# Performance work log

Hardware: AMD Instinct MI355X
Metric: run time of the kernel (lower is better)

Reference implementation:

```python
import jax, jax.numpy as jnp
import numpy as np

NUM_GENES = 5000
EMBED = 64
HID = 64
FEATS = 64
SLOPE = 0.01  # nn.LeakyReLU default
BN_EPS = 1e-5


def setup_inputs() -> dict:
    key = jax.random.key(0)
    ks = jax.random.split(key, 20)
    N, E = 40000, 1280000
    def w(k, shape):
        return jax.random.normal(k, shape, dtype=jnp.float32) * 0.05
    inp = {
        "x": jax.random.normal(ks[0], (N, FEATS), dtype=jnp.float32),
        "edge_index": jax.random.randint(ks[1], (2, E), 0, N, dtype=jnp.int64),
        # pre_mp Linear(num_feats, hidden)
        "W_pre": w(ks[2], (FEATS, HID)), "b_pre": w(ks[3], (HID,)),
        # conv 0 MLP: Linear->LeakyReLU->Linear
        "c0_W1": w(ks[4], (HID, HID)), "c0_b1": w(ks[5], (HID,)),
        "c0_W2": w(ks[6], (HID, HID)), "c0_b2": w(ks[7], (HID,)),
        # bn 0 (only bns[0] is used since last conv has no bn)
        "bn0_g": jnp.ones((HID,), jnp.float32), "bn0_b": jnp.zeros((HID,), jnp.float32),
        # conv 1 MLP
        "c1_W1": w(ks[8], (HID, HID)), "c1_b1": w(ks[9], (HID,)),
        "c1_W2": w(ks[10], (HID, HID)), "c1_b2": w(ks[11], (HID,)),
        # post_mp: Linear(hid,hid)->LeakyReLU->Linear(hid,embed)
        "Wp1": w(ks[12], (HID, HID)), "bp1": w(ks[13], (HID,)),
        "Wp2": w(ks[14], (HID, EMBED)), "bp2": w(ks[15], (EMBED,)),
    }
    return inp


def _gin_conv(x, src, dst, W1, b1, W2, b2):
    # GINConv, eps=0: MLP(x + sum_{j in N(i)} x_j)
    agg = jax.ops.segment_sum(x[src], dst, num_segments=x.shape[0])
    h = x + agg
    h = jax.nn.leaky_relu(h @ W1 + b1, SLOPE) @ W2 + b2
    return h


def _batchnorm(h, g, b):
    mu = h.mean(axis=0)
    var = ((h - mu) ** 2).mean(axis=0)  # biased, training-mode BN
    return (h - mu) * jax.lax.rsqrt(var + BN_EPS) * g + b


def reference(x, edge_index, W_pre, b_pre, c0_W1, c0_b1, c0_W2, c0_b2,
              bn0_g, bn0_b, c1_W1, c1_b1, c1_W2, c1_b2, Wp1, bp1, Wp2, bp2):
    src, dst = edge_index[0], edge_index[1]
    h = x @ W_pre + b_pre                                  # [N, HID]
    h = _gin_conv(h, src, dst, c0_W1, c0_b1, c0_W2, c0_b2)
    h = _batchnorm(h, bn0_g, bn0_b)
    h = _gin_conv(h, src, dst, c1_W1, c1_b1, c1_W2, c1_b2)  # last conv, no bn
    h = jax.nn.leaky_relu(h @ Wp1 + bp1, SLOPE) @ Wp2 + bp2  # [N, EMBED]
    # flatten + split into per-graph chunks of num_genes*embed, then stack
    return h.reshape(-1, NUM_GENES * EMBED)                 # [B, 5000*64]
```

## Files before the change

### kernel.cpp

```cpp
#include <hip/hip_runtime.h>
#include <hip/hip_fp16.h>

constexpr float SLOPE  = 0.01f;
constexpr float BN_EPS = 1e-5f;
constexpr int   CAP    = 96;
constexpr int   CLAMP  = 80;
constexpr int   NXCD   = 8;
constexpr int   EPB    = 2048;
constexpr int   BSH    = 7;
constexpr int   BINN   = 128;
constexpr int   MAXNB  = 320;
constexpr int   RCAP   = 24;
constexpr int   SUBCAP = 768;

__device__ inline void acc8(const uint4& v, float* a) {
    float2 f;
    f = __half22float2(*(const __half2*)&v.x); a[0] += f.x; a[1] += f.y;
    f = __half22float2(*(const __half2*)&v.y); a[2] += f.x; a[3] += f.y;
    f = __half22float2(*(const __half2*)&v.z); a[4] += f.x; a[5] += f.y;
    f = __half22float2(*(const __half2*)&v.w); a[6] += f.x; a[7] += f.y;
}

__global__ void k_linear_h(const float* __restrict__ x, const float* __restrict__ W,
                           const float* __restrict__ bias, __half* __restrict__ H0, int total) {
    int gid = blockIdx.x * blockDim.x + threadIdx.x;
    if (gid >= total) return;
    int n = gid >> 6, f = gid & 63;
    const float* row = x + (size_t)n * 64;
    float acc = bias[f];
#pragma unroll
    for (int k = 0; k < 64; ++k) acc = fmaf(row[k], W[k * 64 + f], acc);
    H0[gid] = __float2half(acc);
}

__global__ void k_binA(const int* __restrict__ src, const int* __restrict__ dst,
                       int* __restrict__ cursors, unsigned int* __restrict__ binArr,
                       int E, int NB) {
    __shared__ int lcnt[MAXNB];
    __shared__ int gb[MAXNB];
    __shared__ unsigned int lrec[MAXNB][RCAP];
    int bid = blockIdx.x, tid = threadIdx.x;
    int xcd = bid & (NXCD - 1);
    for (int i = tid; i < NB; i += 256) lcnt[i] = 0;
    __syncthreads();
    int base = bid * EPB;
#pragma unroll
    for (int i = 0; i < EPB / 256; ++i) {
        int e = base + i * 256 + tid;
        if (e < E) {
            int d = dst[e];
            int s = src[e];
            int bin = d >> BSH;
            unsigned int rec = ((unsigned int)s << BSH) | (unsigned int)(d & (BINN - 1));
            int pos = atomicAdd(&lcnt[bin], 1);
            if (pos < RCAP) lrec[bin][pos] = rec;
        }
    }
    __syncthreads();
    for (int b = tid; b < NB; b += 256) {
        int m = min(lcnt[b], RCAP);
        gb[b] = (m > 0) ? atomicAdd(&cursors[xcd * NB + b], m) : 0;
    }
    __syncthreads();
    int wid = tid >> 6, lane = tid & 63;
    for (int b = wid; b < NB; b += 4) {
        int m = min(lcnt[b], RCAP);
        if (m == 0) continue;
        int gbase = gb[b];
        unsigned int* dp = binArr + ((size_t)(xcd * NB + b)) * SUBCAP;
        for (int i = lane; i < m; i += 64) {
            int p = gbase + i;
            if (p < SUBCAP) dp[p] = lrec[b][i];
        }
    }
}

__global__ void k_binB(const int* __restrict__ cursors, const unsigned int* __restrict__ binArr,
                       int NB, int* __restrict__ cnt, unsigned short* __restrict__ ssrc, int N) {
    __shared__ int lcnt[BINN];
    __shared__ unsigned short lbkt[BINN][CAP];
    int b = blockIdx.x, tid = threadIdx.x;
    if (tid < BINN) lcnt[tid] = 0;
    __syncthreads();
#pragma unroll
    for (int xx = 0; xx < NXCD; ++xx) {
        int m = min(cursors[xx * NB + b], SUBCAP);
        const unsigned int* arr = binArr + ((size_t)(xx * NB + b)) * SUBCAP;
        for (int i = tid; i < m; i += 256) {
            unsigned int rec = arr[i];
            int dl = rec & (BINN - 1);
            int pos = atomicAdd(&lcnt[dl], 1);
            if (pos < CAP) lbkt[dl][pos] = (unsigned short)(rec >> BSH);
        }
    }
    __syncthreads();
    int n0 = b << BSH;
    int nn = min(BINN, N - n0);
    if (nn <= 0) return;
    if (tid < nn) cnt[n0 + tid] = lcnt[tid];
    const unsigned int* lb32 = (const unsigned int*)lbkt;
    unsigned int* gb32 = (unsigned int*)(ssrc + (size_t)n0 * CAP);
    int tot32 = nn * (CAP / 2);
    for (int i = tid; i < tot32; i += 256) gb32[i] = lb32[i];
}

#define GLD(j) \
    uint4 vA##j, vB##j; \
    { int jA = sidx[g][((j) << 4) + sub]; \
      int jB = sidx[g][((j) << 4) + 8 + sub]; \
      vA##j = in16[(size_t)jA * 8 + q]; \
      vB##j = in16[(size_t)jB * 8 + q]; }
#define GACC(j) do { acc8(vA##j, a); acc8(vB##j, a); } while (0)

__device__ inline float mlp_layer_lds(const unsigned int* __restrict__ Ws,
                                      const float* __restrict__ rowp, int lane, float bias) {
    float a = bias;
#pragma unroll
    for (int k0 = 0; k0 < 16; ++k0) {
        float4 r = *(const float4*)&rowp[k0 * 4];
        unsigned int wa = Ws[(2 * k0) * 64 + lane];
        unsigned int wb = Ws[(2 * k0 + 1) * 64 + lane];
        float2 fa = __half22float2(*(const __half2*)&wa);
        float2 fb = __half22float2(*(const __half2*)&wb);
        a = fmaf(r.x, fa.x, a);
        a = fmaf(r.y, fa.y, a);
        a = fmaf(r.z, fb.x, a);
        a = fmaf(r.w, fb.y, a);
    }
    return a;
}

template <bool BN_IN, bool DO_POST, typename TO>
__global__ void k_conv10(const __half* __restrict__ in, const int* __restrict__ cnt,
                         const unsigned short* __restrict__ ssrc,
                         const float* __restrict__ stats, const float* __restrict__ gm,
                         const float* __restrict__ bt, float invN,
                         const float* __restrict__ W1, const float* __restrict__ b1,
                         const float* __restrict__ W2, const float* __restrict__ b2,
                         const float* __restrict__ Wp1, const float* __restrict__ bp1,
                         const float* __restrict__ Wp2, const float* __restrict__ bp2,
                         TO* __restrict__ out, int N, int nblk) {
    constexpr int NMAT = DO_POST ? 4 : 2;
    __shared__ unsigned int Ws[NMAT][2048];
    __shared__ unsigned short sidx[4][CAP];
    __shared__ float row[4][64];
    __shared__ float t[4][64];
    __shared__ float csc[64], csh[64];

    int tid = threadIdx.x;
    {
        const float* mats[NMAT];
        mats[0] = W1; mats[1] = W2;
        if constexpr (DO_POST) { mats[2] = Wp1; mats[3] = Wp2; }
#pragma unroll
        for (int m = 0; m < NMAT; ++m) {
            const float* Wm = mats[m];
#pragma unroll
            for (int it = 0; it < 8; ++it) {
                int idx = it * 256 + tid;
                int k2 = idx >> 6, ln = idx & 63;
                float w0 = Wm[(2 * k2) * 64 + ln];
                float w1 = Wm[(2 * k2 + 1) * 64 + ln];
                __half2 h = __floats2half2_rn(w0, w1);
                Ws[m][idx] = *(unsigned int*)&h;
            }
        }
    }
    if constexpr (BN_IN) {
        if (tid < 64) {
            float mu  = stats[tid] * invN;
            float var = stats[64 + tid] * invN - mu * mu;
            float sc  = rsqrtf(var + BN_EPS) * gm[tid];
            csc[tid] = sc;
            csh[tid] = bt[tid] - mu * sc;
        }
    }
    __syncthreads();

    int bid = blockIdx.x;
    int q8 = nblk / NXCD, r8 = nblk % NXCD;
    int xcd = bid % NXCD, sl = bid / NXCD;
    int wg = (xcd < r8 ? xcd * (q8 + 1) : r8 * (q8 + 1) + (xcd - r8) * q8) + sl;
    int n0 = wg * 4;

    int lane = tid & 63, g = tid >> 6;
    int n = n0 + g;
    bool act = n < N;
    int sub = lane >> 3;
    int q   = lane & 7;

    if (act) {
        const uint4* in16 = (const uint4*)in;
        int c  = min(cnt[n], CLAMP);
        c = __builtin_amdgcn_readfirstlane(c);
        int cp = (c + 15) & ~15;
        int iters = cp >> 4;

        const unsigned short* bkt = ssrc + (size_t)n * CAP;
        unsigned short self = (unsigned short)n;
        if (lane < cp) sidx[g][lane] = (lane < c) ? bkt[lane] : self;
        int p2 = lane + 64;
        if (p2 < cp) sidx[g][p2] = (p2 < c) ? bkt[p2] : self;

        uint4 vs = make_uint4(0, 0, 0, 0);
        if (sub == 0) vs = in16[(size_t)n * 8 + q];

        float a[8] = {0.f, 0.f, 0.f, 0.f, 0.f, 0.f, 0.f, 0.f};
        switch (iters) {
        case 1: { GLD(0) GACC(0); } break;
        case 2: { GLD(0) GLD(1) GACC(0); GACC(1); } break;
        case 3: { GLD(0) GLD(1) GLD(2) GACC(0); GACC(1); GACC(2); } break;
        case 4: { GLD(0) GLD(1) GLD(2) GACC(0); GLD(3) GACC(1); GACC(2); GACC(3); } break;
        case 5: { GLD(0) GLD(1) GLD(2) GACC(0); GLD(3) GACC(1); GLD(4) GACC(2);
                  GACC(3); GACC(4); } break;
        default: break;
        }
#pragma unroll
        for (int k = 0; k < 8; ++k) {
            a[k] += __shfl_xor(a[k], 8);
            a[k] += __shfl_xor(a[k], 16);
            a[k] += __shfl_xor(a[k], 32);
        }
        if (sub == 0) {
            float ws = 1.0f - (float)(cp - c);
            float2 f;
            f = __half22float2(*(const __half2*)&vs.x); a[0] = fmaf(ws, f.x, a[0]); a[1] = fmaf(ws, f.y, a[1]);
            f = __half22float2(*(const __half2*)&vs.y); a[2] = fmaf(ws, f.x, a[2]); a[3] = fmaf(ws, f.y, a[3]);
            f = __half22float2(*(const __half2*)&vs.z); a[4] = fmaf(ws, f.x, a[4]); a[5] = fmaf(ws, f.y, a[5]);
            f = __half22float2(*(const __half2*)&vs.w); a[6] = fmaf(ws, f.x, a[6]); a[7] = fmaf(ws, f.y, a[7]);
            int f0 = q * 8;
            if constexpr (BN_IN) {
                float dp1 = (float)(c + 1);
#pragma unroll
                for (int k = 0; k < 8; ++k) a[k] = fmaf(csc[f0 + k], a[k], dp1 * csh[f0 + k]);
            }
            *(float4*)&row[g][f0]     = make_float4(a[0], a[1], a[2], a[3]);
            *(float4*)&row[g][f0 + 4] = make_float4(a[4], a[5], a[6], a[7]);
        }

        float a1 = mlp_layer_lds(Ws[0], row[g], lane, b1[lane]);
        t[g][lane] = a1 > 0.f ? a1 : SLOPE * a1;

        float a2 = mlp_layer_lds(Ws[1], t[g], lane, b2[lane]);
        if constexpr (!DO_POST) {
            out[(size_t)n * 64 + lane] = (TO)a2;
        } else {
            row[g][lane] = a2;
            float a3 = mlp_layer_lds(Ws[2], row[g], lane, bp1[lane]);
            t[g][lane] = a3 > 0.f ? a3 : SLOPE * a3;
            float a4 = mlp_layer_lds(Ws[3], t[g], lane, bp2[lane]);
            out[(size_t)n * 64 + lane] = (TO)a4;
        }
    }
}

__global__ void k_bn_stats_h(const __half* __restrict__ h, float* __restrict__ stats, int N) {
    int f = threadIdx.x & 63, g = threadIdx.x >> 6;
    float s = 0.f, ss = 0.f;
    for (int r = blockIdx.x * 4 + g; r < N; r += gridDim.x * 4) {
        float v = __half2float(h[(size_t)r * 64 + f]);
        s += v;
        ss += v * v;
    }
    __shared__ float sh[2][256];
    sh[0][threadIdx.x] = s;
    sh[1][threadIdx.x] = ss;
    __syncthreads();
    if (g == 0) {
        s  = sh[0][f] + sh[0][f + 64] + sh[0][f + 128] + sh[0][f + 192];
        ss = sh[1][f] + sh[1][f + 64] + sh[1][f + 128] + sh[1][f + 192];
        atomicAdd(&stats[f], s);
        atomicAdd(&stats[64 + f], ss);
    }
}

__global__ void k_fill_linear(const int* __restrict__ src, const int* __restrict__ dst,
                              int* __restrict__ cnt, unsigned short* __restrict__ ssrc, int E,
                              const float* __restrict__ x, const float* __restrict__ W,
                              const float* __restrict__ bias, __half* __restrict__ H0,
                              int total, int fillBlocks, int N, int Npart) {
    int bid = blockIdx.x;
    if (bid < fillBlocks) {
        int p     = bid & (NXCD - 1);
        int chunk = bid >> 3;
        int lo = p * Npart;
        int hi = min(N, lo + Npart);
        int base = chunk * EPB;
#pragma unroll
        for (int i = 0; i < EPB / 256; ++i) {
            int e = base + i * 256 + (int)threadIdx.x;
            if (e < E) {
                int d = dst[e];
                if (d >= lo && d < hi) {
                    int pos = atomicAdd(&cnt[d], 1);
                    if (pos < CAP) ssrc[(size_t)d * CAP + pos] = (unsigned short)src[e];
                }
            }
        }
    } else {
        int gid = (bid - fillBlocks) * 256 + threadIdx.x;
        if (gid < total) {
            int n = gid >> 6, f = gid & 63;
            const float* row = x + (size_t)n * 64;
            float acc = bias[f];
#pragma unroll
            for (int k = 0; k < 64; ++k) acc = fmaf(row[k], W[k * 64 + f], acc);
            H0[gid] = __float2half(acc);
        }
    }
}

__global__ void k_linear_f(const float* __restrict__ in, const float* __restrict__ W,
                           const float* __restrict__ bias, float* __restrict__ out, int total) {
    int gid = blockIdx.x * blockDim.x + threadIdx.x;
    if (gid >= total) return;
    int n = gid >> 6, f = gid & 63;
    const float* row = in + (size_t)n * 64;
    float acc = bias[f];
#pragma unroll
    for (int k = 0; k < 64; ++k) acc = fmaf(row[k], W[k * 64 + f], acc);
    out[gid] = acc;
}

__global__ void k_scatter(const float* __restrict__ h, const int* __restrict__ src,
                          const int* __restrict__ dst, float* __restrict__ agg, int E) {
    long long gid = (long long)blockIdx.x * blockDim.x + threadIdx.x;
    if (gid >= (long long)E * 64) return;
    int e = (int)(gid >> 6);
    int f = (int)(gid & 63);
    atomicAdd(&agg[(size_t)dst[e] * 64 + f], h[(size_t)src[e] * 64 + f]);
}

__global__ void k_mlp2(const float* __restrict__ in, const float* __restrict__ agg,
                       const float* __restrict__ W1, const float* __restrict__ b1,
                       const float* __restrict__ W2, const float* __restrict__ b2,
                       float* __restrict__ out, int N) {
    __shared__ float row[4][64];
    __shared__ float t[4][64];
    int f = threadIdx.x & 63, g = threadIdx.x >> 6;
    int n = blockIdx.x * 4 + g;
    bool act = n < N;
    if (act) {
        float v = in[(size_t)n * 64 + f];
        if (agg) v += agg[(size_t)n * 64 + f];
        row[g][f] = v;
    }
    __syncthreads();
    if (act) {
        float acc = b1[f];
#pragma unroll
        for (int k = 0; k < 64; ++k) acc = fmaf(row[g][k], W1[k * 64 + f], acc);
        t[g][f] = acc > 0.f ? acc : SLOPE * acc;
    }
    __syncthreads();
    if (act) {
        float acc = b2[f];
#pragma unroll
        for (int k = 0; k < 64; ++k) acc = fmaf(t[g][k], W2[k * 64 + f], acc);
        out[(size_t)n * 64 + f] = acc;
    }
}

__global__ void k_bn_stats_f(const float* __restrict__ h, float* __restrict__ stats, int N) {
    int f = threadIdx.x & 63, g = threadIdx.x >> 6;
    float s = 0.f, ss = 0.f;
    for (int r = blockIdx.x * 4 + g; r < N; r += gridDim.x * 4) {
        float v = h[(size_t)r * 64 + f];
        s += v;
        ss += v * v;
    }
    __shared__ float sh[2][256];
    sh[0][threadIdx.x] = s;
    sh[1][threadIdx.x] = ss;
    __syncthreads();
    if (g == 0) {
        s  = sh[0][f] + sh[0][f + 64] + sh[0][f + 128] + sh[0][f + 192];
        ss = sh[1][f] + sh[1][f + 64] + sh[1][f + 128] + sh[1][f + 192];
        atomicAdd(&stats[f], s);
        atomicAdd(&stats[64 + f], ss);
    }
}

__global__ void k_bn_apply(float* __restrict__ h, const float* __restrict__ stats,
                           const float* __restrict__ gm, const float* __restrict__ bt,
                           int total, float invN) {
    int gid = blockIdx.x * blockDim.x + threadIdx.x;
    if (gid >= total) return;
    int f = gid & 63;
    float mu  = stats[f] * invN;
    float var = stats[64 + f] * invN - mu * mu;
    float sc  = rsqrtf(var + BN_EPS) * gm[f];
    h[gid] = (h[gid] - mu) * sc + bt[f];
}

extern "C" void kernel_launch(void* const* d_in, const int* in_sizes, int n_in,
                              void* d_out, int out_size, void* d_ws, size_t ws_size,
                              hipStream_t stream) {
    const float* x      = (const float*)d_in[0];
    const int*   ei     = (const int*)d_in[1];
    const float* W_pre  = (const float*)d_in[2];
    const float* b_pre  = (const float*)d_in[3];
    const float* c0_W1  = (const float*)d_in[4];
    const float* c0_b1  = (const float*)d_in[5];
    const float* c0_W2  = (const float*)d_in[6];
    const float* c0_b2  = (const float*)d_in[7];
    const float* bn0_g  = (const float*)d_in[8];
    const float* bn0_b  = (const float*)d_in[9];
    const float* c1_W1  = (const float*)d_in[10];
    const float* c1_b1  = (const float*)d_in[11];
    const float* c1_W2  = (const float*)d_in[12];
    const float* c1_b2  = (const float*)d_in[13];
    const float* Wp1    = (const float*)d_in[14];
    const float* bp1    = (const float*)d_in[15];
    const float* Wp2    = (const float*)d_in[16];
    const float* bp2    = (const float*)d_in[17];

    const int N = in_sizes[0] / 64;
    const int E = in_sizes[1] / 2;
    const int total = N * 64;
    const float invN = 1.0f / (float)N;

    const int* src = ei;
    const int* dst = ei + E;

    dim3 blk(256);
    dim3 grid_n((N + 3) / 4);
    int nblk = (N + 3) / 4;
    int linBlocks = (total + 255) / 256;

    const int NB = (N + BINN - 1) / BINN;
    int partBlocks = (E + EPB - 1) / EPB;

    size_t bucketsB = (size_t)N * CAP * 2 + 256;
    size_t cntB     = (size_t)N * 4;
    size_t curB     = (size_t)NXCD * NB * 4;
    size_t binArrB  = (size_t)NXCD * NB * SUBCAP * 4;
    size_t needBin  = (size_t)total * 2 + bucketsB + cntB + 1024 + curB + binArrB + 512;
    size_t needSingle = (size_t)total * 2 + bucketsB + cntB + 1024;

    if (ws_size >= needBin && NB <= MAXNB) {
        char* w = (char*)d_ws;
        __half* H1 = (__half*)w;                     w += (size_t)total * 2;
        unsigned short* ssrc = (unsigned short*)w;   w += bucketsB;
        w = (char*)(((size_t)w + 255) & ~(size_t)255);
        int* cnt = (int*)w;                          w += cntB;
        float* stats = (float*)w;                    w += 512;
        w = (char*)(((size_t)w + 255) & ~(size_t)255);
        int* cursors = (int*)w;                      w += curB;
        w = (char*)(((size_t)w + 255) & ~(size_t)255);
        unsigned int* binArr = (unsigned int*)w;

        __half* H0 = (__half*)d_out;
        hipMemsetAsync(cursors, 0, curB, stream);
        hipMemsetAsync(stats, 0, 128 * 4, stream);
        k_linear_h<<<dim3(linBlocks), blk, 0, stream>>>(x, W_pre, b_pre, H0, total);
        k_binA<<<dim3(partBlocks), blk, 0, stream>>>(src, dst, cursors, binArr, E, NB);
        k_binB<<<dim3(NB), blk, 0, stream>>>(cursors, binArr, NB, cnt, ssrc, N);
        k_conv10<false, false, __half><<<grid_n, blk, 0, stream>>>(
            H0, cnt, ssrc, nullptr, nullptr, nullptr, 0.f,
            c0_W1, c0_b1, c0_W2, c0_b2, nullptr, nullptr, nullptr, nullptr,
            H1, N, nblk);
        k_bn_stats_h<<<dim3(256), blk, 0, stream>>>(H1, stats, N);
        k_conv10<true, true, float><<<grid_n, blk, 0, stream>>>(
            H1, cnt, ssrc, stats, bn0_g, bn0_b, invN,
            c1_W1, c1_b1, c1_W2, c1_b2, Wp1, bp1, Wp2, bp2,
            (float*)d_out, N, nblk);
    } else if (ws_size >= needSingle) {
        char* w = (char*)d_ws;
        __half* H1 = (__half*)w;                     w += (size_t)total * 2;
        unsigned short* ssrc = (unsigned short*)w;   w += bucketsB;
        w = (char*)(((size_t)w + 255) & ~(size_t)255);
        int* cnt = (int*)w;                          w += cntB;
        float* stats = (float*)w;

        int Npart = (N + NXCD - 1) / NXCD;
        int fillBlocks = ((E + EPB - 1) / EPB) * NXCD;
        __half* H0 = (__half*)d_out;
        hipMemsetAsync(cnt, 0, cntB, stream);
        hipMemsetAsync(stats, 0, 128 * 4, stream);
        k_fill_linear<<<dim3(fillBlocks + linBlocks), blk, 0, stream>>>(
            src, dst, cnt, ssrc, E, x, W_pre, b_pre, H0,
            total, fillBlocks, N, Npart);
        k_conv10<false, false, __half><<<grid_n, blk, 0, stream>>>(
            H0, cnt, ssrc, nullptr, nullptr, nullptr, 0.f,
            c0_W1, c0_b1, c0_W2, c0_b2, nullptr, nullptr, nullptr, nullptr,
            H1, N, nblk);
        k_bn_stats_h<<<dim3(256), blk, 0, stream>>>(H1, stats, N);
        k_conv10<true, true, float><<<grid_n, blk, 0, stream>>>(
            H1, cnt, ssrc, stats, bn0_g, bn0_b, invN,
            c1_W1, c1_b1, c1_W2, c1_b2, Wp1, bp1, Wp2, bp2,
            (float*)d_out, N, nblk);
    } else {
        float* A   = (float*)d_out;
        float* B   = (float*)d_ws;
        float* st2 = B + (size_t)total;
        dim3 grid_nf((total + 255) / 256);
        dim3 grid_ef((unsigned)(((long long)E * 64 + 255) / 256));
        k_linear_f<<<grid_nf, blk, 0, stream>>>(x, W_pre, b_pre, A, total);
        hipMemsetAsync(B, 0, (size_t)total * 4, stream);
        k_scatter<<<grid_ef, blk, 0, stream>>>(A, src, dst, B, E);
        k_mlp2<<<grid_n, blk, 0, stream>>>(A, B, c0_W1, c0_b1, c0_W2, c0_b2, A, N);
        hipMemsetAsync(st2, 0, 128 * 4, stream);
        k_bn_stats_f<<<dim3(1024), blk, 0, stream>>>(A, st2, N);
        k_bn_apply<<<grid_nf, blk, 0, stream>>>(A, st2, bn0_g, bn0_b, total, invN);
        hipMemsetAsync(B, 0, (size_t)total * 4, stream);
        k_scatter<<<grid_ef, blk, 0, stream>>>(A, src, dst, B, E);
        k_mlp2<<<grid_n, blk, 0, stream>>>(A, B, c1_W1, c1_b1, c1_W2, c1_b2, A, N);
        k_mlp2<<<grid_n, blk, 0, stream>>>(A, nullptr, Wp1, bp1, Wp2, bp2, A, N);
    }
}
```

Baseline: 209.6 us.

## Fuse BN statistics into conv kernel and use 8-node 512-thread blocks

Removes the separate batch-norm statistics kernel by accumulating per-feature sum and sum-of-squares of the first conv output in shared memory, then issuing one global atomic per feature per block. Blocks grow from 4 to 8 nodes (512 threads), which halves the number of per-block weight-matrix loads into LDS. The statistics are computed from the fp32 values before the fp16 store, which differs slightly from the old path that read the stored halves. Larger blocks with more LDS per block may reduce occupancy.

```diff
diff --git a/kernel.cpp b/kernel.cpp
--- a/kernel.cpp
+++ b/kernel.cpp
@@ -130,22 +130,24 @@
     return a;
 }
 
-template <bool BN_IN, bool DO_POST, typename TO>
-__global__ void k_conv10(const __half* __restrict__ in, const int* __restrict__ cnt,
-                         const unsigned short* __restrict__ ssrc,
-                         const float* __restrict__ stats, const float* __restrict__ gm,
-                         const float* __restrict__ bt, float invN,
-                         const float* __restrict__ W1, const float* __restrict__ b1,
-                         const float* __restrict__ W2, const float* __restrict__ b2,
-                         const float* __restrict__ Wp1, const float* __restrict__ bp1,
-                         const float* __restrict__ Wp2, const float* __restrict__ bp2,
-                         TO* __restrict__ out, int N, int nblk) {
+template <bool BN_IN, bool DO_POST, bool BN_OUT, typename TO>
+__global__ __launch_bounds__(512)
+void k_conv12(const __half* __restrict__ in, const int* __restrict__ cnt,
+              const unsigned short* __restrict__ ssrc,
+              float* __restrict__ stats, const float* __restrict__ gm,
+              const float* __restrict__ bt, float invN,
+              const float* __restrict__ W1, const float* __restrict__ b1,
+              const float* __restrict__ W2, const float* __restrict__ b2,
+              const float* __restrict__ Wp1, const float* __restrict__ bp1,
+              const float* __restrict__ Wp2, const float* __restrict__ bp2,
+              TO* __restrict__ out, int N, int nblk) {
     constexpr int NMAT = DO_POST ? 4 : 2;
     __shared__ unsigned int Ws[NMAT][2048];
-    __shared__ unsigned short sidx[4][CAP];
-    __shared__ float row[4][64];
-    __shared__ float t[4][64];
+    __shared__ unsigned short sidx[8][CAP];
+    __shared__ float row[8][64];
+    __shared__ float t[8][64];
     __shared__ float csc[64], csh[64];
+    __shared__ float bnp[64], bnq[64];
 
     int tid = threadIdx.x;
     {
@@ -156,12 +158,11 @@
         for (int m = 0; m < NMAT; ++m) {
             const float* Wm = mats[m];
 #pragma unroll
-            for (int it = 0; it < 8; ++it) {
-                int idx = it * 256 + tid;
+            for (int it = 0; it < 4; ++it) {
+                int idx = it * 512 + tid;
                 int k2 = idx >> 6, ln = idx & 63;
-                float w0 = Wm[(2 * k2) * 64 + ln];
-                float w1 = Wm[(2 * k2 + 1) * 64 + ln];
-                __half2 h = __floats2half2_rn(w0, w1);
+                __half2 h = __floats2half2_rn(Wm[(2 * k2) * 64 + ln],
+                                              Wm[(2 * k2 + 1) * 64 + ln]);
                 Ws[m][idx] = *(unsigned int*)&h;
             }
         }
@@ -175,13 +176,16 @@
             csh[tid] = bt[tid] - mu * sc;
         }
     }
+    if constexpr (BN_OUT) {
+        if (tid < 64) { bnp[tid] = 0.f; bnq[tid] = 0.f; }
+    }
     __syncthreads();
 
     int bid = blockIdx.x;
     int q8 = nblk / NXCD, r8 = nblk % NXCD;
     int xcd = bid % NXCD, sl = bid / NXCD;
     int wg = (xcd < r8 ? xcd * (q8 + 1) : r8 * (q8 + 1) + (xcd - r8) * q8) + sl;
-    int n0 = wg * 4;
+    int n0 = wg * 8;
 
     int lane = tid & 63, g = tid >> 6;
     int n = n0 + g;
@@ -189,6 +193,7 @@
     int sub = lane >> 3;
     int q   = lane & 7;
 
+    float a2v = 0.f;
     if (act) {
         const uint4* in16 = (const uint4*)in;
         int c  = min(cnt[n], CLAMP);
@@ -242,6 +247,7 @@
         t[g][lane] = a1 > 0.f ? a1 : SLOPE * a1;
 
         float a2 = mlp_layer_lds(Ws[1], t[g], lane, b2[lane]);
+        a2v = a2;
         if constexpr (!DO_POST) {
             out[(size_t)n * 64 + lane] = (TO)a2;
         } else {
@@ -252,25 +258,16 @@
             out[(size_t)n * 64 + lane] = (TO)a4;
         }
     }
-}
-
-__global__ void k_bn_stats_h(const __half* __restrict__ h, float* __restrict__ stats, int N) {
-    int f = threadIdx.x & 63, g = threadIdx.x >> 6;
-    float s = 0.f, ss = 0.f;
-    for (int r = blockIdx.x * 4 + g; r < N; r += gridDim.x * 4) {
-        float v = __half2float(h[(size_t)r * 64 + f]);
-        s += v;
-        ss += v * v;
-    }
-    __shared__ float sh[2][256];
-    sh[0][threadIdx.x] = s;
-    sh[1][threadIdx.x] = ss;
-    __syncthreads();
-    if (g == 0) {
-        s  = sh[0][f] + sh[0][f + 64] + sh[0][f + 128] + sh[0][f + 192];
-        ss = sh[1][f] + sh[1][f + 64] + sh[1][f + 128] + sh[1][f + 192];
-        atomicAdd(&stats[f], s);
-        atomicAdd(&stats[64 + f], ss);
+    if constexpr (BN_OUT) {
+        if (act) {
+            atomicAdd(&bnp[lane], a2v);
+            atomicAdd(&bnq[lane], a2v * a2v);
+        }
+        __syncthreads();
+        if (tid < 64) {
+            atomicAdd(&stats[tid], bnp[tid]);
+            atomicAdd(&stats[64 + tid], bnq[tid]);
+        }
     }
 }
 
@@ -424,8 +421,8 @@
     const int* dst = ei + E;
 
     dim3 blk(256);
-    dim3 grid_n((N + 3) / 4);
-    int nblk = (N + 3) / 4;
+    int nblk8 = (N + 7) / 8;
+    dim3 grid_n8(nblk8);
     int linBlocks = (total + 255) / 256;
 
     const int NB = (N + BINN - 1) / BINN;
@@ -456,15 +453,14 @@
         k_linear_h<<<dim3(linBlocks), blk, 0, stream>>>(x, W_pre, b_pre, H0, total);
         k_binA<<<dim3(partBlocks), blk, 0, stream>>>(src, dst, cursors, binArr, E, NB);
         k_binB<<<dim3(NB), blk, 0, stream>>>(cursors, binArr, NB, cnt, ssrc, N);
-        k_conv10<false, false, __half><<<grid_n, blk, 0, stream>>>(
-            H0, cnt, ssrc, nullptr, nullptr, nullptr, 0.f,
+        k_conv12<false, false, true, __half><<<grid_n8, dim3(512), 0, stream>>>(
+            H0, cnt, ssrc, stats, nullptr, nullptr, 0.f,
             c0_W1, c0_b1, c0_W2, c0_b2, nullptr, nullptr, nullptr, nullptr,
-            H1, N, nblk);
-        k_bn_stats_h<<<dim3(256), blk, 0, stream>>>(H1, stats, N);
-        k_conv10<true, true, float><<<grid_n, blk, 0, stream>>>(
+            H1, N, nblk8);
+        k_conv12<true, true, false, float><<<grid_n8, dim3(512), 0, stream>>>(
             H1, cnt, ssrc, stats, bn0_g, bn0_b, invN,
             c1_W1, c1_b1, c1_W2, c1_b2, Wp1, bp1, Wp2, bp2,
-            (float*)d_out, N, nblk);
+            (float*)d_out, N, nblk8);
     } else if (ws_size >= needSingle) {
         char* w = (char*)d_ws;
         __half* H1 = (__half*)w;                     w += (size_t)total * 2;
@@ -481,31 +477,31 @@
         k_fill_linear<<<dim3(fillBlocks + linBlocks), blk, 0, stream>>>(
             src, dst, cnt, ssrc, E, x, W_pre, b_pre, H0,
             total, fillBlocks, N, Npart);
-        k_conv10<false, false, __half><<<grid_n, blk, 0, stream>>>(
-            H0, cnt, ssrc, nullptr, nullptr, nullptr, 0.f,
+        k_conv12<false, false, true, __half><<<grid_n8, dim3(512), 0, stream>>>(
+            H0, cnt, ssrc, stats, nullptr, nullptr, 0.f,
             c0_W1, c0_b1, c0_W2, c0_b2, nullptr, nullptr, nullptr, nullptr,
-            H1, N, nblk);
-        k_bn_stats_h<<<dim3(256), blk, 0, stream>>>(H1, stats, N);
-        k_conv10<true, true, float><<<grid_n, blk, 0, stream>>>(
+            H1, N, nblk8);
+        k_conv12<true, true, false, float><<<grid_n8, dim3(512), 0, stream>>>(
             H1, cnt, ssrc, stats, bn0_g, bn0_b, invN,
             c1_W1, c1_b1, c1_W2, c1_b2, Wp1, bp1, Wp2, bp2,
-            (float*)d_out, N, nblk);
+            (float*)d_out, N, nblk8);
     } else {
         float* A   = (float*)d_out;
         float* B   = (float*)d_ws;
         float* st2 = B + (size_t)total;
         dim3 grid_nf((total + 255) / 256);
+        dim3 grid_n4((N + 3) / 4);
         dim3 grid_ef((unsigned)(((long long)E * 64 + 255) / 256));
         k_linear_f<<<grid_nf, blk, 0, stream>>>(x, W_pre, b_pre, A, total);
         hipMemsetAsync(B, 0, (size_t)total * 4, stream);
         k_scatter<<<grid_ef, blk, 0, stream>>>(A, src, dst, B, E);
-        k_mlp2<<<grid_n, blk, 0, stream>>>(A, B, c0_W1, c0_b1, c0_W2, c0_b2, A, N);
+        k_mlp2<<<grid_n4, blk, 0, stream>>>(A, B, c0_W1, c0_b1, c0_W2, c0_b2, A, N);
         hipMemsetAsync(st2, 0, 128 * 4, stream);
         k_bn_stats_f<<<dim3(1024), blk, 0, stream>>>(A, st2, N);
         k_bn_apply<<<grid_nf, blk, 0, stream>>>(A, st2, bn0_g, bn0_b, total, invN);
         hipMemsetAsync(B, 0, (size_t)total * 4, stream);
         k_scatter<<<grid_ef, blk, 0, stream>>>(A, src, dst, B, E);
-        k_mlp2<<<grid_n, blk, 0, stream>>>(A, B, c1_W1, c1_b1, c1_W2, c1_b2, A, N);
-        k_mlp2<<<grid_n, blk, 0, stream>>>(A, nullptr, Wp1, bp1, Wp2, bp2, A, N);
-    }
-}
+        k_mlp2<<<grid_n4, blk, 0, stream>>>(A, B, c1_W1, c1_b1, c1_W2, c1_b2, A, N);
+        k_mlp2<<<grid_n4, blk, 0, stream>>>(A, nullptr, Wp1, bp1, Wp2, bp2, A, N);
+    }
+}
```

Result: slower. 282.1 us (+34.6%).
